# Optimization experiments

Measured on AMD Instinct MI355X. Metric: run time of the kernel, lower is better.

## Reference

```python
import jax, jax.numpy as jnp
import numpy as np

NEG_SLOPE = 0.01  # F.leaky_relu default
N_NODES = 50000
N_EDGES = 800000
DIMS = [1, 64, 128, 64, 1]


def _lrelu(x):
    return jnp.where(x >= 0, x, NEG_SLOPE * x)


def _gconv(x, src, dst, W, b, n):
    # DGL GraphConv, norm='none': sum-aggregate src features into dst, then linear.
    # (DGL multiplies first when in_feats > out_feats; identical math since sum is linear.)
    if x.shape[1] > W.shape[1]:
        x = x @ W
        return jax.ops.segment_sum(x[src], dst, num_segments=n) + b
    agg = jax.ops.segment_sum(x[src], dst, num_segments=n)  # [n, d_in]
    return agg @ W + b


def setup_inputs() -> dict:
    key = jax.random.key(0)
    ks = jax.random.split(key, 16)
    inp = {
        "in_feat": jax.random.normal(ks[0], (N_NODES, 1), jnp.float32),
        "src": jax.random.randint(ks[1], (N_EDGES,), 0, N_NODES),
        "dst": jax.random.randint(ks[2], (N_EDGES,), 0, N_NODES),
    }
    for i in range(4):
        fi, fo = DIMS[i], DIMS[i + 1]
        scale = (2.0 / (fi + fo)) ** 0.5  # xavier-style
        inp[f"W{i}"] = jax.random.normal(ks[3 + 2 * i], (fi, fo), jnp.float32) * scale
        inp[f"b{i}"] = jax.random.normal(ks[4 + 2 * i], (fo,), jnp.float32) * 0.01
    return inp


def reference(in_feat, src, dst, W0, b0, W1, b1, W2, b2, W3, b3):
    n = in_feat.shape[0]
    h = _lrelu(_gconv(in_feat, src, dst, W0, b0, n))
    h = _lrelu(_gconv(h, src, dst, W1, b1, n))
    h = _lrelu(_gconv(h, src, dst, W2, b2, n))
    h = _lrelu(_gconv(h, src, dst, W3, b3, n))
    return h[1]  # node index 1, shape (1,)
```

## Files before the change

### kernel.cpp

```cpp
#include <hip/hip_runtime.h>

#define N_NODES 50000
#define N_EDGES 800000
#define NE4 (N_EDGES / 4)
#define NMASKW 1568
#define C1MAX 64
#define CAP   16
#define S2MAX 1024
#define DMAX  4096
#define BK    96
#define SB1   ((NE4 + 255) / 256)
#define FGRID 256

#define AS(p, v)  __hip_atomic_store((p), (v), __ATOMIC_RELAXED, __HIP_MEMORY_SCOPE_AGENT)

__device__ __forceinline__ float lrelu(float v) { return v >= 0.f ? v : 0.01f * v; }
__device__ __forceinline__ bool mtest(const unsigned int* m, int i) {
    return (m[i >> 5] >> (i & 31)) & 1u;
}

__global__ __launch_bounds__(256) void scan1_k(const int4* __restrict__ dst4,
                                               const int* __restrict__ src,
                                               int* __restrict__ e1cnt, int* __restrict__ e1val,
                                               unsigned int* __restrict__ zbase, int zwords) {
    __shared__ int lcnt;
    __shared__ int lval[CAP];
    const int tid = threadIdx.x;
    const int t = blockIdx.x * 256 + tid;
    if (tid == 0) lcnt = 0;
    __syncthreads();
    if (t < zwords) zbase[t] = 0u;
    if (t < NE4) {
        int4 d4 = dst4[t];
        int dv[4] = { d4.x, d4.y, d4.z, d4.w };
#pragma unroll
        for (int k = 0; k < 4; ++k) {
            if (dv[k] == 1) {
                int q = atomicAdd(&lcnt, 1);
                if (q < CAP) lval[q] = src[t * 4 + k];
            }
        }
    }
    __syncthreads();
    int c = lcnt < CAP ? lcnt : CAP;
    if (tid == 0) e1cnt[blockIdx.x] = c;
    if (tid < c) e1val[blockIdx.x * CAP + tid] = lval[tid];
}

__global__ __launch_bounds__(256) void scan2_k(const int4* __restrict__ dst4,
                                               const int* __restrict__ src,
                                               const int* __restrict__ e1cnt,
                                               const int* __restrict__ e1val,
                                               unsigned int* __restrict__ f2m,
                                               int* __restrict__ pos2, int* __restrict__ cnt2,
                                               int2* __restrict__ eD, int* __restrict__ cntD,
                                               int* __restrict__ mult, int* __restrict__ cnt1g) {
    __shared__ unsigned int msk[NMASKW];
    __shared__ int candN[C1MAX];
    __shared__ int candC;
    const int tid = threadIdx.x;
    for (int k = tid; k < NMASKW; k += 256) msk[k] = 0u;
    if (tid == 0) candC = 0;
    __syncthreads();
    for (int b = tid; b < SB1; b += 256) {
        int c = e1cnt[b]; if (c > CAP) c = CAP;
        for (int i = 0; i < c; ++i) {
            int n = e1val[b * CAP + i];
            unsigned int bit = 1u << (n & 31);
            unsigned int old = atomicOr(&msk[n >> 5], bit);
            if (!(old & bit)) { int q = atomicAdd(&candC, 1); if (q < C1MAX) candN[q] = n; }
        }
    }
    __syncthreads();
    int c1 = candC; if (c1 > C1MAX) c1 = C1MAX;
    if (blockIdx.x == 0 && tid == 0) AS(cnt1g, c1);
    int t = blockIdx.x * 256 + tid;
    if (t >= NE4) return;
    int4 d4 = dst4[t];
    int dv[4] = { d4.x, d4.y, d4.z, d4.w };
#pragma unroll
    for (int k = 0; k < 4; ++k) {
        int dd = dv[k];
        if (dd == 1) {
            int ss = src[t * 4 + k];
            int r = 0;
            for (int u = 0; u < c1; ++u) r += (candN[u] < ss);
            atomicAdd(&mult[r], 1);
        }
        if (mtest(msk, dd)) {
            int ss = src[t * 4 + k];
            unsigned int bit = 1u << (ss & 31);
            unsigned int old = atomicOr(&f2m[ss >> 5], bit);
            if (!(old & bit)) {
                int q2 = atomicAdd(cnt2, 1);
                if (q2 < S2MAX) AS(&pos2[ss], q2);
            }
            int r = 0;
            for (int u = 0; u < c1; ++u) r += (candN[u] < dd);
            int q = atomicAdd(cntD, 1);
            if (q < DMAX) {
                unsigned long long ev = (unsigned long long)(unsigned int)ss |
                                        ((unsigned long long)(unsigned int)r << 32);
                AS((unsigned long long*)&eD[q], ev);
            }
        }
    }
}

__global__ __launch_bounds__(256) void scan3_k(const int4* __restrict__ dst4,
                                               const int* __restrict__ src,
                                               const unsigned int* __restrict__ f2m,
                                               unsigned int* __restrict__ f3m,
                                               const int* __restrict__ pos2,
                                               float* __restrict__ agg0,
                                               int* __restrict__ bucket,
                                               int* __restrict__ slotCnt) {
    __shared__ unsigned int msk[NMASKW];
    const int tid = threadIdx.x;
    for (int k = tid; k < NMASKW; k += 256) msk[k] = f2m[k];
    __syncthreads();
    int t = blockIdx.x * 256 + tid;
    if (t >= NE4) return;
    int4 d4 = dst4[t];
    int dv[4] = { d4.x, d4.y, d4.z, d4.w };
#pragma unroll
    for (int k = 0; k < 4; ++k) {
        int dd = dv[k];
        if (mtest(msk, dd)) {
            int ss = src[t * 4 + k];
            unsigned int bit = 1u << (ss & 31);
            unsigned int old = atomicOr(&f3m[ss >> 5], bit);
            if (!(old & bit)) AS(&agg0[ss], 0.f);
            int sl = pos2[dd];
            if ((unsigned)sl < S2MAX) {
                int bi = atomicAdd(&slotCnt[sl], 1);
                if (bi < BK) AS(&bucket[sl * BK + bi], ss);
            }
        }
    }
}

__global__ __launch_bounds__(256) void scan4_k(const int4* __restrict__ dst4,
                                               const int4* __restrict__ src4,
                                               const float* __restrict__ x,
                                               const unsigned int* __restrict__ f3m,
                                               float* __restrict__ agg0,
                                               const int2* __restrict__ eD,
                                               const int* __restrict__ cntD,
                                               const int* __restrict__ pos2,
                                               int2* __restrict__ eDr) {
    __shared__ unsigned int msk[NMASKW];
    int g = blockIdx.x * 256 + threadIdx.x;
    {
        int cD = *cntD; if (cD > DMAX) cD = DMAX;
        if (g < cD) {
            int2 e = eD[g];
            int sl = pos2[e.x];
            unsigned long long ev =
                (unsigned long long)(unsigned int)((unsigned)sl < S2MAX ? sl : -1) |
                ((unsigned long long)(unsigned int)e.y << 32);
            AS((unsigned long long*)&eDr[g], ev);
        }
    }
    for (int k = threadIdx.x; k < NMASKW; k += 256) msk[k] = f3m[k];
    __syncthreads();
    if (g >= NE4) return;
    int4 d4 = dst4[g];
    bool m0 = mtest(msk, d4.x), m1 = mtest(msk, d4.y);
    bool m2 = mtest(msk, d4.z), m3 = mtest(msk, d4.w);
    if (m0 | m1 | m2 | m3) {
        int4 s4 = src4[g];
        if (m0) atomicAdd(&agg0[d4.x], x[s4.x]);
        if (m1) atomicAdd(&agg0[d4.y], x[s4.y]);
        if (m2) atomicAdd(&agg0[d4.z], x[s4.z]);
        if (m3) atomicAdd(&agg0[d4.w], x[s4.w]);
    }
}

struct PS {
    const int* bucket; const int* slotCnt; const float* agg0;
    const float* W0; const float* b0; const float* W1; const float* b1; const float* W2;
    const int* cnt2; const int2* eDr; const int* cntD;
    float* gacc;
};

__global__ __launch_bounds__(256) void slots_k(PS p) {
    __shared__ float xv[128];
    __shared__ float part[256];
    __shared__ float rowA[64];
    __shared__ float rowH[128];
    __shared__ float rowT[64];
    const int tid = threadIdx.x;
    const int g = tid >> 6, j = tid & 63;
    int c2 = *p.cnt2; if (c2 > S2MAX) c2 = S2MAX;
    int cD = *p.cntD; if (cD > DMAX) cD = DMAX;
    const float w0 = p.W0[j], bb0 = p.b0[j];

    for (int b = blockIdx.x; b < c2; b += FGRID) {
        int2 e0 = make_int2(-1, -1);
        if (tid < cD) e0 = p.eDr[tid];
        int cnt = p.slotCnt[b]; if (cnt > BK) cnt = BK;
        if (tid < cnt) xv[tid] = p.agg0[p.bucket[b * BK + tid]];
        __syncthreads();
        float racc = 0.f;
        for (int m = g; m < cnt; m += 4) racc += lrelu(xv[m] * w0 + bb0);
        part[tid] = racc;
        __syncthreads();
        if (tid < 64)
            rowA[tid] = part[tid] + part[64 + tid] + part[128 + tid] + part[192 + tid];
        __syncthreads();
        if (tid < 128) {
            float h = p.b1[tid];
#pragma unroll
            for (int k = 0; k < 64; ++k) h += rowA[k] * p.W1[k * 128 + tid];
            rowH[tid] = lrelu(h);
        }
        __syncthreads();
        if (tid < 64) {
            float a2 = 0.f;
#pragma unroll
            for (int k = 0; k < 128; ++k) a2 += rowH[k] * p.W2[k * 64 + tid];
            rowT[tid] = a2;
        }
        __syncthreads();
        for (int base = 0; base < cD; base += 256) {
            int i = base + tid;
            int2 e = (base == 0) ? e0 : make_int2(-1, -1);
            if (base != 0 && i < cD) e = p.eDr[i];
            bool m = (e.x == b);
            unsigned long long bal = __ballot(m);
            while (bal) {
                int bit = __builtin_ctzll(bal); bal &= bal - 1;
                int sl1 = __shfl(e.y, bit, 64);
                if ((unsigned)sl1 < C1MAX)
                    atomicAdd(&p.gacc[sl1 * 64 + j], rowT[j]);
            }
        }
        __syncthreads();
    }
}

__global__ __launch_bounds__(256) void tail_k(const float* __restrict__ gacc,
                                              const int* __restrict__ mult,
                                              const int* __restrict__ cnt1g,
                                              const float* __restrict__ b2,
                                              const float* __restrict__ W3,
                                              const float* __restrict__ b3,
                                              float* __restrict__ out) {
    __shared__ float t3s[C1MAX];
    const int tid = threadIdx.x, j = tid & 63, w = tid >> 6;
    int c1 = *cnt1g; if (c1 > C1MAX) c1 = C1MAX;
    for (int r = w; r < c1; r += 4) {
        float v = lrelu(gacc[r * 64 + j] + b2[j]) * W3[j];
        for (int off = 32; off > 0; off >>= 1) v += __shfl_down(v, off, 64);
        if (j == 0) t3s[r] = v;
    }
    __syncthreads();
    if (tid == 0) {
        float s = 0.f;
        for (int r = 0; r < c1; ++r) s += (float)mult[r] * t3s[r];
        out[0] = lrelu(s + b3[0]);
    }
}

extern "C" void kernel_launch(void* const* d_in, const int* in_sizes, int n_in,
                              void* d_out, int out_size, void* d_ws, size_t ws_size,
                              hipStream_t stream) {
    const float* x   = (const float*)d_in[0];
    const int*   src = (const int*)d_in[1];
    const int*   dst = (const int*)d_in[2];
    const float* W0 = (const float*)d_in[3];  const float* b0 = (const float*)d_in[4];
    const float* W1 = (const float*)d_in[5];  const float* b1 = (const float*)d_in[6];
    const float* W2 = (const float*)d_in[7];  const float* b2 = (const float*)d_in[8];
    const float* W3 = (const float*)d_in[9];  const float* b3 = (const float*)d_in[10];
    float* out = (float*)d_out;
    const int4* dst4 = (const int4*)dst;
    const int4* src4 = (const int4*)src;

    char* base = (char*)d_ws;
    size_t off = 0;
    auto take = [&](size_t bytes) { char* q = base + off; off += (bytes + 255) & ~(size_t)255; return q; };
    unsigned int* f2m = (unsigned int*)take(NMASKW * 4);
    unsigned int* f3m = (unsigned int*)take(NMASKW * 4);
    int* cnt2  = (int*)take(4);
    int* cntD  = (int*)take(4);
    int* cnt1g = (int*)take(4);
    int* mult  = (int*)take((size_t)C1MAX * 4);
    int* slotCnt = (int*)take((size_t)S2MAX * 4);
    float* gacc  = (float*)take((size_t)C1MAX * 64 * 4);
    int zwords = (int)(off / 4);
    float* agg0   = (float*)take((size_t)N_NODES * 4);
    int*   e1cnt  = (int*)take((size_t)SB1 * 4);
    int*   e1val  = (int*)take((size_t)SB1 * CAP * 4);
    int2*  eD     = (int2*)take((size_t)DMAX * 8);
    int2*  eDr    = (int2*)take((size_t)DMAX * 8);
    int*   bucket = (int*)take((size_t)S2MAX * BK * 4);
    int*   pos2   = (int*)take((size_t)N_NODES * 4);

    scan1_k<<<SB1, 256, 0, stream>>>(dst4, src, e1cnt, e1val, (unsigned int*)base, zwords);
    scan2_k<<<SB1, 256, 0, stream>>>(dst4, src, e1cnt, e1val, f2m, pos2, cnt2, eD, cntD,
                                     mult, cnt1g);
    scan3_k<<<SB1, 256, 0, stream>>>(dst4, src, f2m, f3m, pos2, agg0, bucket, slotCnt);
    scan4_k<<<SB1, 256, 0, stream>>>(dst4, src4, x, f3m, agg0, eD, cntD, pos2, eDr);

    PS hp;
    hp.bucket = bucket; hp.slotCnt = slotCnt; hp.agg0 = agg0;
    hp.W0 = W0; hp.b0 = b0; hp.W1 = W1; hp.b1 = b1; hp.W2 = W2;
    hp.cnt2 = cnt2; hp.eDr = eDr; hp.cntD = cntD; hp.gacc = gacc;
    slots_k<<<FGRID, 256, 0, stream>>>(hp);

    tail_k<<<1, 256, 0, stream>>>(gacc, mult, cnt1g, b2, W3, b3, out);
}
```

Baseline: 128.2 us.

## Fuse scan3/scan4 via grid barrier and fold tail into last slots block

Merges the third and fourth edge-scan kernels into one persistent kernel with a fixed grid of 512 blocks. The blocks use a grid-strided loop and a hierarchical atomic counter barrier between the two phases. The tail reduction moves into the slots kernel, where the last block to finish (found by a two-level atomic counter) computes the output. Slot loads are also prefetched before the loop. The aim is to remove two kernel launches and their serialization gaps. The cost is that the spin barrier only works if all 512 blocks are co-resident, and each block now does more serial work.

```diff
diff --git a/kernel.cpp b/kernel.cpp
--- a/kernel.cpp
+++ b/kernel.cpp
@@ -10,9 +10,13 @@
 #define DMAX  4096
 #define BK    96
 #define SB1   ((NE4 + 255) / 256)
+#define G34   512
 #define FGRID 256
+#define SUBW  64
 
 #define AS(p, v)  __hip_atomic_store((p), (v), __ATOMIC_RELAXED, __HIP_MEMORY_SCOPE_AGENT)
+#define ALD(p)    __hip_atomic_load((p), __ATOMIC_RELAXED, __HIP_MEMORY_SCOPE_AGENT)
+#define AADD(p,v) __hip_atomic_fetch_add((p), (v), __ATOMIC_RELAXED, __HIP_MEMORY_SCOPE_AGENT)
 
 __device__ __forceinline__ float lrelu(float v) { return v >= 0.f ? v : 0.01f * v; }
 __device__ __forceinline__ bool mtest(const unsigned int* m, int i) {
@@ -107,81 +111,93 @@
     }
 }
 
-__global__ __launch_bounds__(256) void scan3_k(const int4* __restrict__ dst4,
-                                               const int* __restrict__ src,
-                                               const unsigned int* __restrict__ f2m,
-                                               unsigned int* __restrict__ f3m,
-                                               const int* __restrict__ pos2,
-                                               float* __restrict__ agg0,
-                                               int* __restrict__ bucket,
-                                               int* __restrict__ slotCnt) {
+__global__ __launch_bounds__(256) void scan34_k(const int4* __restrict__ dst4,
+                                                const int* __restrict__ src,
+                                                const int4* __restrict__ src4,
+                                                const float* __restrict__ x,
+                                                const unsigned int* __restrict__ f2m,
+                                                unsigned int* __restrict__ f3m,
+                                                const int* __restrict__ pos2,
+                                                float* __restrict__ agg0,
+                                                int* __restrict__ bucket,
+                                                int* __restrict__ slotCnt,
+                                                const int2* __restrict__ eD,
+                                                const int* __restrict__ cntD,
+                                                int2* __restrict__ eDr,
+                                                int* __restrict__ sub, int* __restrict__ top,
+                                                int* __restrict__ rel) {
     __shared__ unsigned int msk[NMASKW];
     const int tid = threadIdx.x;
+    const int gid = blockIdx.x * 256 + tid;
+    const int T = G34 * 256;
+
     for (int k = tid; k < NMASKW; k += 256) msk[k] = f2m[k];
     __syncthreads();
-    int t = blockIdx.x * 256 + tid;
-    if (t >= NE4) return;
-    int4 d4 = dst4[t];
-    int dv[4] = { d4.x, d4.y, d4.z, d4.w };
-#pragma unroll
-    for (int k = 0; k < 4; ++k) {
-        int dd = dv[k];
-        if (mtest(msk, dd)) {
-            int ss = src[t * 4 + k];
-            unsigned int bit = 1u << (ss & 31);
-            unsigned int old = atomicOr(&f3m[ss >> 5], bit);
-            if (!(old & bit)) AS(&agg0[ss], 0.f);
-            int sl = pos2[dd];
-            if ((unsigned)sl < S2MAX) {
-                int bi = atomicAdd(&slotCnt[sl], 1);
-                if (bi < BK) AS(&bucket[sl * BK + bi], ss);
-            }
-        }
-    }
-}
-
-__global__ __launch_bounds__(256) void scan4_k(const int4* __restrict__ dst4,
-                                               const int4* __restrict__ src4,
-                                               const float* __restrict__ x,
-                                               const unsigned int* __restrict__ f3m,
-                                               float* __restrict__ agg0,
-                                               const int2* __restrict__ eD,
-                                               const int* __restrict__ cntD,
-                                               const int* __restrict__ pos2,
-                                               int2* __restrict__ eDr) {
-    __shared__ unsigned int msk[NMASKW];
-    int g = blockIdx.x * 256 + threadIdx.x;
+    for (int t = gid; t < NE4; t += T) {
+        int4 d4 = dst4[t];
+        int dv[4] = { d4.x, d4.y, d4.z, d4.w };
+#pragma unroll
+        for (int k = 0; k < 4; ++k) {
+            int dd = dv[k];
+            if (mtest(msk, dd)) {
+                int ss = src[t * 4 + k];
+                unsigned int bit = 1u << (ss & 31);
+                unsigned int old = atomicOr(&f3m[ss >> 5], bit);
+                if (!(old & bit)) AS(&agg0[ss], 0.f);
+                int sl = pos2[dd];
+                if ((unsigned)sl < S2MAX) {
+                    int bi = atomicAdd(&slotCnt[sl], 1);
+                    if (bi < BK) AS(&bucket[sl * BK + bi], ss);
+                }
+            }
+        }
+    }
+    __syncthreads();
+    if (tid == 0) {
+        int s = blockIdx.x & 7;
+        int old = AADD(&sub[s * SUBW], 1);
+        if (old == (G34 / 8) - 1) {
+            int o2 = AADD(top, 1);
+            if (o2 == 7) AS(rel, 1);
+        }
+        while (ALD(rel) == 0) __builtin_amdgcn_s_sleep(8);
+    }
+    __syncthreads();
+
     {
         int cD = *cntD; if (cD > DMAX) cD = DMAX;
-        if (g < cD) {
-            int2 e = eD[g];
+        if (gid < cD) {
+            int2 e = eD[gid];
             int sl = pos2[e.x];
             unsigned long long ev =
                 (unsigned long long)(unsigned int)((unsigned)sl < S2MAX ? sl : -1) |
                 ((unsigned long long)(unsigned int)e.y << 32);
-            AS((unsigned long long*)&eDr[g], ev);
-        }
-    }
-    for (int k = threadIdx.x; k < NMASKW; k += 256) msk[k] = f3m[k];
-    __syncthreads();
-    if (g >= NE4) return;
-    int4 d4 = dst4[g];
-    bool m0 = mtest(msk, d4.x), m1 = mtest(msk, d4.y);
-    bool m2 = mtest(msk, d4.z), m3 = mtest(msk, d4.w);
-    if (m0 | m1 | m2 | m3) {
-        int4 s4 = src4[g];
-        if (m0) atomicAdd(&agg0[d4.x], x[s4.x]);
-        if (m1) atomicAdd(&agg0[d4.y], x[s4.y]);
-        if (m2) atomicAdd(&agg0[d4.z], x[s4.z]);
-        if (m3) atomicAdd(&agg0[d4.w], x[s4.w]);
+            AS((unsigned long long*)&eDr[gid], ev);
+        }
+    }
+    for (int k = tid; k < NMASKW; k += 256) msk[k] = f3m[k];
+    __syncthreads();
+    for (int t = gid; t < NE4; t += T) {
+        int4 d4 = dst4[t];
+        bool m0 = mtest(msk, d4.x), m1 = mtest(msk, d4.y);
+        bool m2 = mtest(msk, d4.z), m3 = mtest(msk, d4.w);
+        if (m0 | m1 | m2 | m3) {
+            int4 s4 = src4[t];
+            if (m0) atomicAdd(&agg0[d4.x], x[s4.x]);
+            if (m1) atomicAdd(&agg0[d4.y], x[s4.y]);
+            if (m2) atomicAdd(&agg0[d4.z], x[s4.z]);
+            if (m3) atomicAdd(&agg0[d4.w], x[s4.w]);
+        }
     }
 }
 
 struct PS {
     const int* bucket; const int* slotCnt; const float* agg0;
     const float* W0; const float* b0; const float* W1; const float* b1; const float* W2;
+    const float* b2; const float* W3; const float* b3;
     const int* cnt2; const int2* eDr; const int* cntD;
-    float* gacc;
+    const int* mult; const int* cnt1g;
+    float* gacc; int* subD; int* topD; float* out;
 };
 
 __global__ __launch_bounds__(256) void slots_k(PS p) {
@@ -190,17 +206,25 @@
     __shared__ float rowA[64];
     __shared__ float rowH[128];
     __shared__ float rowT[64];
+    __shared__ float t3s[C1MAX];
+    __shared__ int lflag;
     const int tid = threadIdx.x;
     const int g = tid >> 6, j = tid & 63;
-    int c2 = *p.cnt2; if (c2 > S2MAX) c2 = S2MAX;
-    int cD = *p.cntD; if (cD > DMAX) cD = DMAX;
+    int c2 = *p.cnt2;
+    int cD = *p.cntD;
+    int myCnt0 = p.slotCnt[blockIdx.x];
+    int bidx0 = (tid < BK) ? p.bucket[blockIdx.x * BK + tid] : 0;
+    int2 e0 = (tid < DMAX) ? p.eDr[tid] : make_int2(-1, -1);
+    if (c2 > S2MAX) c2 = S2MAX;
+    if (cD > DMAX) cD = DMAX;
     const float w0 = p.W0[j], bb0 = p.b0[j];
 
     for (int b = blockIdx.x; b < c2; b += FGRID) {
-        int2 e0 = make_int2(-1, -1);
-        if (tid < cD) e0 = p.eDr[tid];
-        int cnt = p.slotCnt[b]; if (cnt > BK) cnt = BK;
-        if (tid < cnt) xv[tid] = p.agg0[p.bucket[b * BK + tid]];
+        int cnt = (b == (int)blockIdx.x) ? myCnt0 : p.slotCnt[b];
+        if (cnt > BK) cnt = BK;
+        int bidx = (b == (int)blockIdx.x) ? bidx0
+                 : ((tid < BK) ? p.bucket[b * BK + tid] : 0);
+        if (tid < cnt) xv[tid] = p.agg0[bidx];
         __syncthreads();
         float racc = 0.f;
         for (int m = g; m < cnt; m += 4) racc += lrelu(xv[m] * w0 + bb0);
@@ -227,7 +251,7 @@
             int i = base + tid;
             int2 e = (base == 0) ? e0 : make_int2(-1, -1);
             if (base != 0 && i < cD) e = p.eDr[i];
-            bool m = (e.x == b);
+            bool m = (e.x == b) && (i < cD);
             unsigned long long bal = __ballot(m);
             while (bal) {
                 int bit = __builtin_ctzll(bal); bal &= bal - 1;
@@ -238,28 +262,34 @@
         }
         __syncthreads();
     }
-}
-
-__global__ __launch_bounds__(256) void tail_k(const float* __restrict__ gacc,
-                                              const int* __restrict__ mult,
-                                              const int* __restrict__ cnt1g,
-                                              const float* __restrict__ b2,
-                                              const float* __restrict__ W3,
-                                              const float* __restrict__ b3,
-                                              float* __restrict__ out) {
-    __shared__ float t3s[C1MAX];
-    const int tid = threadIdx.x, j = tid & 63, w = tid >> 6;
-    int c1 = *cnt1g; if (c1 > C1MAX) c1 = C1MAX;
-    for (int r = w; r < c1; r += 4) {
-        float v = lrelu(gacc[r * 64 + j] + b2[j]) * W3[j];
-        for (int off = 32; off > 0; off >>= 1) v += __shfl_down(v, off, 64);
-        if (j == 0) t3s[r] = v;
-    }
+
     __syncthreads();
     if (tid == 0) {
-        float s = 0.f;
-        for (int r = 0; r < c1; ++r) s += (float)mult[r] * t3s[r];
-        out[0] = lrelu(s + b3[0]);
+        lflag = 0;
+        int s = blockIdx.x & 7;
+        int old = AADD(&p.subD[s * SUBW], 1);
+        if (old == (FGRID / 8) - 1) {
+            int o2 = AADD(p.topD, 1);
+            lflag = (o2 == 7);
+        }
+    }
+    __syncthreads();
+    if (!lflag) return;
+
+    {
+        int c1 = *p.cnt1g; if (c1 > C1MAX) c1 = C1MAX;
+        int w = tid >> 6;
+        for (int r = w; r < c1; r += 4) {
+            float v = lrelu(p.gacc[r * 64 + j] + p.b2[j]) * p.W3[j];
+            for (int off = 32; off > 0; off >>= 1) v += __shfl_down(v, off, 64);
+            if (j == 0) t3s[r] = v;
+        }
+        __syncthreads();
+        if (tid == 0) {
+            float s = 0.f;
+            for (int r = 0; r < c1; ++r) s += (float)p.mult[r] * t3s[r];
+            p.out[0] = lrelu(s + p.b3[0]);
+        }
     }
 }
 
@@ -286,6 +316,11 @@
     int* cntD  = (int*)take(4);
     int* cnt1g = (int*)take(4);
     int* mult  = (int*)take((size_t)C1MAX * 4);
+    int* sub   = (int*)take((size_t)8 * SUBW * 4);
+    int* top   = (int*)take(4);
+    int* rel   = (int*)take(4);
+    int* subD  = (int*)take((size_t)8 * SUBW * 4);
+    int* topD  = (int*)take(4);
     int* slotCnt = (int*)take((size_t)S2MAX * 4);
     float* gacc  = (float*)take((size_t)C1MAX * 64 * 4);
     int zwords = (int)(off / 4);
@@ -300,14 +335,15 @@
     scan1_k<<<SB1, 256, 0, stream>>>(dst4, src, e1cnt, e1val, (unsigned int*)base, zwords);
     scan2_k<<<SB1, 256, 0, stream>>>(dst4, src, e1cnt, e1val, f2m, pos2, cnt2, eD, cntD,
                                      mult, cnt1g);
-    scan3_k<<<SB1, 256, 0, stream>>>(dst4, src, f2m, f3m, pos2, agg0, bucket, slotCnt);
-    scan4_k<<<SB1, 256, 0, stream>>>(dst4, src4, x, f3m, agg0, eD, cntD, pos2, eDr);
+    scan34_k<<<G34, 256, 0, stream>>>(dst4, src, src4, x, f2m, f3m, pos2, agg0,
+                                      bucket, slotCnt, eD, cntD, eDr, sub, top, rel);
 
     PS hp;
     hp.bucket = bucket; hp.slotCnt = slotCnt; hp.agg0 = agg0;
     hp.W0 = W0; hp.b0 = b0; hp.W1 = W1; hp.b1 = b1; hp.W2 = W2;
-    hp.cnt2 = cnt2; hp.eDr = eDr; hp.cntD = cntD; hp.gacc = gacc;
+    hp.b2 = b2; hp.W3 = W3; hp.b3 = b3;
+    hp.cnt2 = cnt2; hp.eDr = eDr; hp.cntD = cntD;
+    hp.mult = mult; hp.cnt1g = cnt1g;
+    hp.gacc = gacc; hp.subD = subD; hp.topD = topD; hp.out = out;
     slots_k<<<FGRID, 256, 0, stream>>>(hp);
-
-    tail_k<<<1, 256, 0, stream>>>(gacc, mult, cnt1g, b2, W3, b3, out);
-}
+}
```

Measured after the change: 129.7 us. About the same (+1.1%).
